# Kernel optimization log

Measured on AMD Instinct MI355X. Metric: run time of the kernel, lower is better.

## Reference

```python
import jax, jax.numpy as jnp
import numpy as np

EPS = 1e-5  # torch LayerNorm default

def _layer_norm(v, w, b):
    mu = jnp.mean(v, axis=-1, keepdims=True)
    var = jnp.mean(jnp.square(v - mu), axis=-1, keepdims=True)
    return (v - mu) * jax.lax.rsqrt(var + EPS) * w + b

def _gru_layer(x, h0, w_ih, b_ih, w_hh, b_hh, ln_w, ln_b):
    # x: [B,T,in], h0: [B,H]
    H = h0.shape[-1]
    # precompute input gates for whole sequence: [B,T,3H]
    x_gates = jnp.einsum('bti,gi->btg', x, w_ih) + b_ih

    def step(h, xg_t):
        hg = jnp.einsum('bh,gh->bg', h, w_hh) + b_hh
        x_r, x_z, x_n = jnp.split(xg_t, 3, axis=-1)
        h_r, h_z, h_n = jnp.split(hg, 3, axis=-1)
        r = jax.nn.sigmoid(_layer_norm(x_r + h_r, ln_w[0], ln_b[0]))
        z = jax.nn.sigmoid(_layer_norm(x_z + h_z, ln_w[1], ln_b[1]))
        n = jnp.tanh(_layer_norm(x_n + r * h_n, ln_w[2], ln_b[2]))
        h_new = (1 - z) * n + z * h
        return h_new, h_new

    h_final, ys = jax.lax.scan(step, h0, jnp.swapaxes(x_gates, 0, 1))
    return jnp.swapaxes(ys, 0, 1), h_final  # [B,T,H], [B,H]

def setup_inputs() -> dict:
    key = jax.random.key(0)
    ks = jax.random.split(key, 4)
    B, T, D, H, L = 64, 512, 768, 768, 2
    G = 3 * H
    x = jax.random.normal(ks[0], (B, T, D), dtype=jnp.float32)
    h_0 = jnp.zeros((L, B, H), dtype=jnp.float32)
    # scaled gaussian stands in for orthogonal init
    w_ih = jax.random.normal(ks[1], (L, G, D), dtype=jnp.float32) / np.sqrt(D)
    w_hh = jax.random.normal(ks[2], (L, G, H), dtype=jnp.float32) / np.sqrt(H)
    b_ih = jnp.zeros((L, G), dtype=jnp.float32)
    b_hh = jnp.zeros((L, G), dtype=jnp.float32)
    ln_w = jnp.ones((L, 3, H), dtype=jnp.float32)
    ln_b = jnp.zeros((L, 3, H), dtype=jnp.float32)
    return {"x": x, "h_0": h_0, "w_ih": w_ih, "b_ih": b_ih,
            "w_hh": w_hh, "b_hh": b_hh, "ln_w": ln_w, "ln_b": ln_b}

def reference(x, h_0, w_ih, b_ih, w_hh, b_hh, ln_w, ln_b):
    num_layers = h_0.shape[0]
    layer_output = x
    x_residual = x  # input_size == hidden_size -> identity residual
    finals = []
    for i in range(num_layers):
        seq, h_fin = _gru_layer(layer_output, h_0[i], w_ih[i], b_ih[i],
                                w_hh[i], b_hh[i], ln_w[i], ln_b[i])
        if i == 0:
            seq = seq + x_residual
        else:
            seq = seq + layer_output
        layer_output = seq  # dropout=0.0, eval mode -> no-op
        finals.append(h_fin)
    h_final_stack = jnp.stack(finals, axis=0)
    return layer_output, h_final_stack
```

## Files before the change

kernel.cpp:

```cpp
#include <hip/hip_runtime.h>

typedef short bf16x8 __attribute__((ext_vector_type(8)));
typedef float f32x4 __attribute__((ext_vector_type(4)));

__device__ __forceinline__ unsigned pack2bf(float a, float b) {
  union { float f; unsigned u; } x, y;
  x.f = a; y.f = b;
  unsigned ra = (x.u + 0x7FFFu + ((x.u >> 16) & 1u)) >> 16;
  unsigned rb = (y.u + 0x7FFFu + ((y.u >> 16) & 1u)) & 0xFFFF0000u;
  return ra | rb;
}
__device__ __forceinline__ unsigned short bfu(float f) {
  union { float f; unsigned u; } v; v.f = f;
  return (unsigned short)((v.u + 0x7FFFu + ((v.u >> 16) & 1u)) >> 16);
}
__device__ __forceinline__ float sigf(float x) { return 1.f / (1.f + __expf(-x)); }

#define KB 64
#define LDSP 72

__global__ __launch_bounds__(256) void gemm_bt(
    const float* __restrict__ A0, size_t a_bstride,
    const float* __restrict__ W,
    const float* __restrict__ bias,
    float* __restrict__ out, size_t o_bstride,
    int Mvalid)
{
  __shared__ unsigned short As[64][LDSP];
  __shared__ unsigned short Bs[64][LDSP];
  const int tid = threadIdx.x;
  const int g0 = blockIdx.x * 64;
  const int mlo = blockIdx.z * 64;
  const float* Ab = A0 + (size_t)blockIdx.y * a_bstride + (size_t)mlo * 768;
  float* outb = out + (size_t)blockIdx.y * o_bstride + (size_t)mlo * 2304;

  const int srow = tid >> 2;
  const int scol = (tid & 3) << 4;
  const int wv = tid >> 6;
  const int lane = tid & 63;
  const int wr = wv >> 1, wc = wv & 1;
  const int lrow = lane & 15;
  const int lk = (lane >> 4) << 3;

  f32x4 acc[2][2];
#pragma unroll
  for (int i = 0; i < 2; ++i)
#pragma unroll
    for (int j = 0; j < 2; ++j)
      acc[i][j] = (f32x4){0.f, 0.f, 0.f, 0.f};

  const float* Aptr = Ab + (size_t)srow * 768 + scol;
  const float* Bptr = W + ((size_t)(g0 + srow)) * 768 + scol;
  const bool aval = (mlo + srow) < Mvalid;

  for (int k0 = 0; k0 < 768; k0 += KB) {
    uint4 ua0, ua1, ub0, ub1;
    if (aval) {
      const float4* qa = (const float4*)(Aptr + k0);
      float4 f0 = qa[0], f1 = qa[1], f2 = qa[2], f3 = qa[3];
      ua0 = make_uint4(pack2bf(f0.x, f0.y), pack2bf(f0.z, f0.w),
                       pack2bf(f1.x, f1.y), pack2bf(f1.z, f1.w));
      ua1 = make_uint4(pack2bf(f2.x, f2.y), pack2bf(f2.z, f2.w),
                       pack2bf(f3.x, f3.y), pack2bf(f3.z, f3.w));
    } else {
      ua0 = make_uint4(0u, 0u, 0u, 0u);
      ua1 = ua0;
    }
    {
      const float4* qb = (const float4*)(Bptr + k0);
      float4 f0 = qb[0], f1 = qb[1], f2 = qb[2], f3 = qb[3];
      ub0 = make_uint4(pack2bf(f0.x, f0.y), pack2bf(f0.z, f0.w),
                       pack2bf(f1.x, f1.y), pack2bf(f1.z, f1.w));
      ub1 = make_uint4(pack2bf(f2.x, f2.y), pack2bf(f2.z, f2.w),
                       pack2bf(f3.x, f3.y), pack2bf(f3.z, f3.w));
    }
    __syncthreads();
    *(uint4*)&As[srow][scol] = ua0;
    *(uint4*)&As[srow][scol + 8] = ua1;
    *(uint4*)&Bs[srow][scol] = ub0;
    *(uint4*)&Bs[srow][scol + 8] = ub1;
    __syncthreads();
#pragma unroll
    for (int kh = 0; kh < 2; ++kh) {
      bf16x8 a0 = *(const bf16x8*)&As[32 * wr + lrow][32 * kh + lk];
      bf16x8 a1 = *(const bf16x8*)&As[32 * wr + 16 + lrow][32 * kh + lk];
      bf16x8 b0 = *(const bf16x8*)&Bs[32 * wc + lrow][32 * kh + lk];
      bf16x8 b1 = *(const bf16x8*)&Bs[32 * wc + 16 + lrow][32 * kh + lk];
      acc[0][0] = __builtin_amdgcn_mfma_f32_16x16x32_bf16(a0, b0, acc[0][0], 0, 0, 0);
      acc[0][1] = __builtin_amdgcn_mfma_f32_16x16x32_bf16(a0, b1, acc[0][1], 0, 0, 0);
      acc[1][0] = __builtin_amdgcn_mfma_f32_16x16x32_bf16(a1, b0, acc[1][0], 0, 0, 0);
      acc[1][1] = __builtin_amdgcn_mfma_f32_16x16x32_bf16(a1, b1, acc[1][1], 0, 0, 0);
    }
  }

  const int lgrp = lane >> 4;
#pragma unroll
  for (int fr = 0; fr < 2; ++fr)
#pragma unroll
    for (int fc = 0; fc < 2; ++fc)
#pragma unroll
      for (int j = 0; j < 4; ++j) {
        int m = 32 * wr + 16 * fr + lgrp * 4 + j;
        int n = 32 * wc + 16 * fc + lrow;
        if (mlo + m < Mvalid)
          outb[(size_t)m * 2304 + g0 + n] = acc[fr][fc][j] + bias[g0 + n];
      }
}

#define NWGP 72
#define NWGC 64
#define NWGT 136
#define EPS 1e-5f
#define INV768 (1.0f / 768.0f)
#define SLOT 24576u

__device__ __forceinline__ void bar_arrive(unsigned* c) {
  __syncthreads();
  if (threadIdx.x == 0)
    __hip_atomic_fetch_add(c + (blockIdx.x & 7) * 32, 1u,
                           __ATOMIC_RELAXED, __HIP_MEMORY_SCOPE_AGENT);
}
__device__ __forceinline__ void bar_wait(unsigned* c, unsigned tgt) {
  if (threadIdx.x == 0) {
    for (;;) {
      unsigned s = 0;
#pragma unroll
      for (int i = 0; i < 8; ++i)
        s += __hip_atomic_load(c + i * 32, __ATOMIC_RELAXED, __HIP_MEMORY_SCOPE_AGENT);
      if (s >= tgt) break;
      __builtin_amdgcn_s_sleep(1);
    }
  }
  __syncthreads();
}

template <int N>
__device__ __forceinline__ void blk_reduce(float* v, float* lds) {
#pragma unroll
  for (int k = 0; k < N; ++k) {
    float x = v[k];
#pragma unroll
    for (int off = 1; off < 64; off <<= 1) x += __shfl_xor(x, off);
    v[k] = x;
  }
  const int wv = threadIdx.x >> 6;
  const int lane = threadIdx.x & 63;
  if (lane == 0) {
#pragma unroll
    for (int k = 0; k < N; ++k) lds[wv * N + k] = v[k];
  }
  __syncthreads();
#pragma unroll
  for (int k = 0; k < N; ++k)
    v[k] = lds[k] + lds[N + k] + lds[2 * N + k] + lds[3 * N + k];
  __syncthreads();
}

#define WAITV(n) do { asm volatile("s_waitcnt vmcnt(" #n ")" ::: "memory"); \
                      __builtin_amdgcn_sched_barrier(0); } while (0)

#define LD24(buf, base) \
  { _Pragma("unroll") for (int kk_ = 0; kk_ < 24; ++kk_) { \
      const unsigned* p_ = (base) + (size_t)kk_ * 1024u; \
      asm volatile("global_load_dwordx4 %0, %1, off sc0 sc1" : "=v"(buf[kk_]) : "v"(p_)); } }

#define WRRING(ring, t, val) \
  { unsigned* rp_ = (ring) + (unsigned)(((t) & 3)) * SLOT; \
    _Pragma("unroll") for (int p_ = 0; p_ < 3; ++p_) { \
      int i_ = tid + (p_ << 8); \
      float other_ = __shfl_xor(val[p_], 1); \
      if ((tid & 1) == 0) { \
        unsigned pk_ = pack2bf(val[p_], other_); \
        __hip_atomic_store(rp_ + (i_ >> 3) * 256 + b * 4 + ((i_ >> 1) & 3), pk_, \
                           __ATOMIC_RELAXED, __HIP_MEMORY_SCOPE_AGENT); } } }

__global__ __launch_bounds__(256, 1) void gru_super(
    const float* __restrict__ Whh1, const float* __restrict__ bhh1,
    const float* __restrict__ Wih2, const float* __restrict__ bih2,
    const float* __restrict__ Whh2, const float* __restrict__ bhh2,
    const float* __restrict__ lnw, const float* __restrict__ lnb,
    const float* __restrict__ x,
    const float* __restrict__ xg1,
    int t0, int TC,
    const float* __restrict__ h0,
    float* __restrict__ hstate,
    unsigned* __restrict__ h1ring, unsigned* __restrict__ s1ring,
    unsigned* __restrict__ h2ring,
    float* __restrict__ hg1, float* __restrict__ xg2, float* __restrict__ hg2,
    unsigned* __restrict__ bar,
    float* __restrict__ seq,
    float* __restrict__ hfin,
    int firstflag, int lastflag)
{
  __shared__ unsigned short Wl[96][776];
  __shared__ float bl96[96];
  __shared__ float redl[32];

  unsigned* barA = bar;
  unsigned* barB = bar + 512;

  const int wg = blockIdx.x;
  const int tid = threadIdx.x;
  const int lane = tid & 63;
  const int w = tid >> 6;
  const int la = lane & 15;
  const int kb = lane >> 4;
  const int arow = 16 * w + la;

  if (wg < NWGP) {
    const int mcls = wg / 24;
    const int g0w = (wg % 24) * 96;
    const unsigned abase = (unsigned)((kb * 64 + arow) << 2);
    {
      const float* Wsrc = (mcls == 0) ? Whh1 : (mcls == 1) ? Wih2 : Whh2;
      const float* bsrc = (mcls == 0) ? bhh1 : (mcls == 1) ? bih2 : bhh2;
      for (int r = 0; r < 96; ++r) {
        const float* src = Wsrc + (size_t)(g0w + r) * 768;
        for (int c = tid; c < 768; c += 256) Wl[r][c] = bfu(src[c]);
      }
      if (tid < 96) bl96[tid] = bsrc[g0w + tid];
    }
    float* dst = (mcls == 0) ? hg1 : (mcls == 1) ? xg2 : hg2;

    for (int s = 0; s <= TC; ++s) {
      const int t1 = t0 + s;
      const bool active = (mcls == 0) ? (s < TC) : (s >= 1);
      bar_wait(barB, 64u * (unsigned)(s + 1));
      if (active) {
        const unsigned* rbase =
            (mcls == 0) ? (h1ring + (unsigned)((t1 - 1) & 3) * SLOT)
          : (mcls == 1) ? (s1ring + (unsigned)((t1 - 1) & 3) * SLOT)
                        : (h2ring + (unsigned)((t1 - 2) & 3) * SLOT);
        const unsigned* hb = rbase + abase;
        f32x4 acc[6];
#pragma unroll
        for (int r = 0; r < 6; ++r) acc[r] = (f32x4){0.f, 0.f, 0.f, 0.f};
        bf16x8 buf[24];
        LD24(buf, hb);
        WAITV(0);
#pragma unroll
        for (int kk = 0; kk < 24; ++kk) {
#pragma unroll
          for (int r = 0; r < 6; ++r) {
            bf16x8 wv2 = *(const bf16x8*)&Wl[16 * r + la][kk * 32 + kb * 8];
            acc[r] = __builtin_amdgcn_mfma_f32_16x16x32_bf16(buf[kk], wv2, acc[r], 0, 0, 0);
          }
        }
#pragma unroll
        for (int r = 0; r < 6; ++r)
#pragma unroll
          for (int j = 0; j < 4; ++j) {
            int bb = 16 * w + kb * 4 + j;
            __hip_atomic_store(dst + (size_t)bb * 2304 + g0w + 16 * r + la,
                               acc[r][j] + bl96[16 * r + la],
                               __ATOMIC_RELAXED, __HIP_MEMORY_SCOPE_AGENT);
          }
      }
      bar_arrive(barA);
    }
    return;
  }

  const int b = wg - NWGP;
  float hreg1[3], hreg2[3];
  float h1prev[3], xprev[3] = {0.f, 0.f, 0.f}, xcur[3] = {0.f, 0.f, 0.f};
  float lw1[9], lb1[9], lw2[9], lb2[9];
#pragma unroll
  for (int g = 0; g < 3; ++g)
#pragma unroll
    for (int p = 0; p < 3; ++p) {
      int idx = g * 3 + p, gi = g * 768 + tid + (p << 8);
      lw1[idx] = lnw[gi];          lb1[idx] = lnb[gi];
      lw2[idx] = lnw[2304 + gi];   lb2[idx] = lnb[2304 + gi];
    }
#pragma unroll
  for (int p = 0; p < 3; ++p) {
    int i = tid + (p << 8);
    hreg1[p] = firstflag ? h0[(size_t)b * 768 + i] : hstate[(size_t)b * 768 + i];
    hreg2[p] = firstflag ? h0[49152 + (size_t)b * 768 + i] : hstate[49152 + (size_t)b * 768 + i];
    h1prev[p] = hreg1[p];
  }
  if (firstflag) {
    WRRING(h1ring, 3, hreg1);
    WRRING(h2ring, 3, hreg2);
  }
  bar_arrive(barB);

  for (int s = 0; s <= TC; ++s) {
    const int t1 = t0 + s;
    const bool doL1 = (s < TC);
    const bool doL2 = (s >= 1);

    const int ttc = doL1 ? s : (TC - 1);
    float x1v[9];
    {
      const float* xg1b = xg1 + ((size_t)b * TC + ttc) * 2304;
#pragma unroll
      for (int p = 0; p < 9; ++p) x1v[p] = xg1b[tid + p * 256];
    }
    if (doL1) {
#pragma unroll
      for (int p = 0; p < 3; ++p)
        xcur[p] = x[((size_t)b * 512 + t1) * 768 + tid + (p << 8)];
    }

    bar_wait(barA, 72u * (unsigned)(s + 1));

    float g1v[9], g2v[9], g3v[9];
    {
      const float* p1 = hg1 + (size_t)b * 2304;
      const float* p2 = xg2 + (size_t)b * 2304;
      const float* p3 = hg2 + (size_t)b * 2304;
#pragma unroll
      for (int p = 0; p < 9; ++p) {
        const float* q1 = p1 + tid + p * 256;
        const float* q2 = p2 + tid + p * 256;
        const float* q3 = p3 + tid + p * 256;
        asm volatile("global_load_dword %0, %1, off sc0 sc1" : "=v"(g1v[p]) : "v"(q1));
        asm volatile("global_load_dword %0, %1, off sc0 sc1" : "=v"(g2v[p]) : "v"(q2));
        asm volatile("global_load_dword %0, %1, off sc0 sc1" : "=v"(g3v[p]) : "v"(q3));
      }
    }
    WAITV(0);

    float s11[3], s21[3], s12[3], s22[3];
    float v8[8] = {0,0,0,0,0,0,0,0};
#pragma unroll
    for (int p = 0; p < 3; ++p) {
      s11[p] = g1v[p] + x1v[p];
      s21[p] = g1v[3 + p] + x1v[3 + p];
      s12[p] = g2v[p] + g3v[p];
      s22[p] = g2v[3 + p] + g3v[3 + p];
      v8[0] += s11[p]; v8[1] += s11[p] * s11[p];
      v8[2] += s21[p]; v8[3] += s21[p] * s21[p];
      v8[4] += s12[p]; v8[5] += s12[p] * s12[p];
      v8[6] += s22[p]; v8[7] += s22[p] * s22[p];
    }
    blk_reduce<8>(v8, redl);
    float mu11 = v8[0] * INV768, rs11 = rsqrtf(v8[1] * INV768 - mu11 * mu11 + EPS);
    float mu21 = v8[2] * INV768, rs21 = rsqrtf(v8[3] * INV768 - mu21 * mu21 + EPS);
    float mu12 = v8[4] * INV768, rs12 = rsqrtf(v8[5] * INV768 - mu12 * mu12 + EPS);
    float mu22 = v8[6] * INV768, rs22 = rsqrtf(v8[7] * INV768 - mu22 * mu22 + EPS);

    float z1[3], m1[3], z2[3], m2[3];
    float v4[4] = {0,0,0,0};
#pragma unroll
    for (int p = 0; p < 3; ++p) {
      float r1 = sigf((s11[p] - mu11) * rs11 * lw1[p] + lb1[p]);
      z1[p]    = sigf((s21[p] - mu21) * rs21 * lw1[3 + p] + lb1[3 + p]);
      m1[p] = x1v[6 + p] + r1 * g1v[6 + p];
      float r2 = sigf((s12[p] - mu12) * rs12 * lw2[p] + lb2[p]);
      z2[p]    = sigf((s22[p] - mu22) * rs22 * lw2[3 + p] + lb2[3 + p]);
      m2[p] = g2v[6 + p] + r2 * g3v[6 + p];
      v4[0] += m1[p]; v4[1] += m1[p] * m1[p];
      v4[2] += m2[p]; v4[3] += m2[p] * m2[p];
    }
    blk_reduce<4>(v4, redl);
    float mum1 = v4[0] * INV768, rsm1 = rsqrtf(v4[1] * INV768 - mum1 * mum1 + EPS);
    float mum2 = v4[2] * INV768, rsm2 = rsqrtf(v4[3] * INV768 - mum2 * mum2 + EPS);

    float h1new[3], s1new[3], h2new[3], seqv[3];
#pragma unroll
    for (int p = 0; p < 3; ++p) {
      float n1 = tanhf((m1[p] - mum1) * rsm1 * lw1[6 + p] + lb1[6 + p]);
      h1new[p] = (1.f - z1[p]) * n1 + z1[p] * hreg1[p];
      s1new[p] = h1new[p] + xcur[p];
      float n2 = tanhf((m2[p] - mum2) * rsm2 * lw2[6 + p] + lb2[6 + p]);
      h2new[p] = (1.f - z2[p]) * n2 + z2[p] * hreg2[p];
    }
    if (doL2) {
#pragma unroll
      for (int p = 0; p < 3; ++p) {
        hreg2[p] = h2new[p];
        seqv[p] = h2new[p] + h1prev[p] + xprev[p];
      }
      WRRING(h2ring, t1 - 1, h2new);
    }
    if (doL1) {
#pragma unroll
      for (int p = 0; p < 3; ++p) {
        hreg1[p] = h1new[p];
        h1prev[p] = h1new[p];
        xprev[p] = xcur[p];
      }
      WRRING(h1ring, t1, h1new);
      WRRING(s1ring, t1, s1new);
    }
    bar_arrive(barB);
    if (doL2) {
      const int t2 = t1 - 1;
#pragma unroll
      for (int p = 0; p < 3; ++p) {
        int i = tid + (p << 8);
        seq[((size_t)b * 512 + t2) * 768 + i] = seqv[p];
      }
    }
  }

#pragma unroll
  for (int p = 0; p < 3; ++p) {
    int i = tid + (p << 8);
    hstate[(size_t)b * 768 + i] = hreg1[p];
    hstate[49152 + (size_t)b * 768 + i] = hreg2[p];
    if (lastflag) {
      hfin[(size_t)b * 768 + i] = hreg1[p];
      hfin[49152 + (size_t)b * 768 + i] = hreg2[p];
    }
  }
}

extern "C" void kernel_launch(void* const* d_in, const int* in_sizes, int n_in,
                              void* d_out, int out_size, void* d_ws, size_t ws_size,
                              hipStream_t stream) {
  const float* x    = (const float*)d_in[0];
  const float* h0   = (const float*)d_in[1];
  const float* w_ih = (const float*)d_in[2];
  const float* b_ih = (const float*)d_in[3];
  const float* w_hh = (const float*)d_in[4];
  const float* b_hh = (const float*)d_in[5];
  const float* lnw  = (const float*)d_in[6];
  const float* lnb  = (const float*)d_in[7];
  float* out = (float*)d_out;

  const int B = 64, T = 512, H = 768, G = 2304;

  const size_t BAR = 65536;
  const size_t RING = 4u * SLOT * 4u;
  const size_t HGB = (size_t)B * G * 4;
  int CHUNK = 128;
  for (;;) {
    size_t need = BAR + 3 * RING + 3 * HGB + 2 * (size_t)B * H * 4
                + (size_t)B * CHUNK * G * 4;
    if (need <= ws_size || CHUNK == 8) break;
    CHUNK >>= 1;
  }

  char* wp = (char*)d_ws;
  unsigned* barctr = (unsigned*)wp;            wp += BAR;
  unsigned* h1ring = (unsigned*)wp;            wp += RING;
  unsigned* s1ring = (unsigned*)wp;            wp += RING;
  unsigned* h2ring = (unsigned*)wp;            wp += RING;
  float* hg1 = (float*)wp;                     wp += HGB;
  float* xg2 = (float*)wp;                     wp += HGB;
  float* hg2 = (float*)wp;                     wp += HGB;
  float* hstate = (float*)wp;                  wp += 2 * (size_t)B * H * 4;
  float* xg1 = (float*)wp;

  hipMemsetAsync(barctr, 0, BAR, stream);

  float* seq  = out;
  float* hfin = out + (size_t)B * T * H;
  const int NCH = T / CHUNK;

  const float* Wih1 = w_ih;
  const float* Wih2 = w_ih + (size_t)G * H;
  const float* Whh1 = w_hh;
  const float* Whh2 = w_hh + (size_t)G * H;

  for (int c = 0; c < NCH; ++c) {
    int t0 = c * CHUNK;
    gemm_bt<<<dim3(G / 64, B, CHUNK / 64), 256, 0, stream>>>(
        x + (size_t)t0 * H, (size_t)T * H, Wih1, b_ih,
        xg1, (size_t)CHUNK * G, CHUNK);
    gru_super<<<NWGT, 256, 0, stream>>>(
        Whh1, b_hh, Wih2, b_ih + G, Whh2, b_hh + G,
        lnw, lnb, x, xg1, t0, CHUNK,
        h0, hstate, h1ring, s1ring, h2ring,
        hg1, xg2, hg2,
        barctr + (size_t)c * 1024,
        seq, hfin,
        (c == 0) ? 1 : 0, (c == NCH - 1) ? 1 : 0);
  }
}
```

Before: 6.639 ms.

## Split layer-1 and layer-2 cell workgroups into separate per-batch blocks

The persistent kernel now launches 200 workgroups. The 64 cell workgroups that each handled both layers for one batch row become 128: 64 handle layer 1 and 64 handle layer 2, and the barrier target rises to 128 arrivals. Each cell block now runs half the elementwise and LayerNorm work per step with smaller reductions, which should shorten the critical path between the grid barriers. In exchange, layer-2 blocks read the layer-1 output plus residual back from the bf16 s1ring instead of summing fp32 values in registers, which lowers precision of the residual, and more blocks take part in each barrier.

```diff
diff --git a/kernel.cpp b/kernel.cpp
--- a/kernel.cpp
+++ b/kernel.cpp
@@ -13,6 +13,9 @@
 __device__ __forceinline__ unsigned short bfu(float f) {
   union { float f; unsigned u; } v; v.f = f;
   return (unsigned short)((v.u + 0x7FFFu + ((v.u >> 16) & 1u)) >> 16);
+}
+__device__ __forceinline__ float u2f(unsigned u) {
+  union { unsigned u; float f; } v; v.u = u; return v.f;
 }
 __device__ __forceinline__ float sigf(float x) { return 1.f / (1.f + __expf(-x)); }
 
@@ -107,9 +110,7 @@
       }
 }
 
-#define NWGP 72
-#define NWGC 64
-#define NWGT 136
+#define NWGT 200
 #define EPS 1e-5f
 #define INV768 (1.0f / 768.0f)
 #define SLOT 24576u
@@ -207,7 +208,7 @@
   const int kb = lane >> 4;
   const int arow = 16 * w + la;
 
-  if (wg < NWGP) {
+  if (wg < 72) {
     const int mcls = wg / 24;
     const int g0w = (wg % 24) * 96;
     const unsigned abase = (unsigned)((kb * 64 + arow) << 2);
@@ -224,8 +225,10 @@
 
     for (int s = 0; s <= TC; ++s) {
       const int t1 = t0 + s;
-      const bool active = (mcls == 0) ? (s < TC) : (s >= 1);
-      bar_wait(barB, 64u * (unsigned)(s + 1));
+      const bool doL1 = (s < TC);
+      const bool doL2 = (s >= 1);
+      const bool active = (mcls == 0) ? doL1 : doL2;
+      bar_wait(barB, 128u * (unsigned)(s + 1));
       if (active) {
         const unsigned* rbase =
             (mcls == 0) ? (h1ring + (unsigned)((t1 - 1) & 3) * SLOT)
@@ -234,25 +237,25 @@
         const unsigned* hb = rbase + abase;
         f32x4 acc[6];
 #pragma unroll
-        for (int r = 0; r < 6; ++r) acc[r] = (f32x4){0.f, 0.f, 0.f, 0.f};
+        for (int q = 0; q < 6; ++q) acc[q] = (f32x4){0.f, 0.f, 0.f, 0.f};
         bf16x8 buf[24];
         LD24(buf, hb);
         WAITV(0);
 #pragma unroll
         for (int kk = 0; kk < 24; ++kk) {
 #pragma unroll
-          for (int r = 0; r < 6; ++r) {
-            bf16x8 wv2 = *(const bf16x8*)&Wl[16 * r + la][kk * 32 + kb * 8];
-            acc[r] = __builtin_amdgcn_mfma_f32_16x16x32_bf16(buf[kk], wv2, acc[r], 0, 0, 0);
+          for (int q = 0; q < 6; ++q) {
+            bf16x8 wv2 = *(const bf16x8*)&Wl[16 * q + la][kk * 32 + kb * 8];
+            acc[q] = __builtin_amdgcn_mfma_f32_16x16x32_bf16(buf[kk], wv2, acc[q], 0, 0, 0);
           }
         }
 #pragma unroll
-        for (int r = 0; r < 6; ++r)
+        for (int q = 0; q < 6; ++q)
 #pragma unroll
           for (int j = 0; j < 4; ++j) {
             int bb = 16 * w + kb * 4 + j;
-            __hip_atomic_store(dst + (size_t)bb * 2304 + g0w + 16 * r + la,
-                               acc[r][j] + bl96[16 * r + la],
+            __hip_atomic_store(dst + (size_t)bb * 2304 + g0w + 16 * q + la,
+                               acc[q][j] + bl96[16 * q + la],
                                __ATOMIC_RELAXED, __HIP_MEMORY_SCOPE_AGENT);
           }
       }
@@ -261,150 +264,201 @@
     return;
   }
 
-  const int b = wg - NWGP;
-  float hreg1[3], hreg2[3];
-  float h1prev[3], xprev[3] = {0.f, 0.f, 0.f}, xcur[3] = {0.f, 0.f, 0.f};
-  float lw1[9], lb1[9], lw2[9], lb2[9];
-#pragma unroll
-  for (int g = 0; g < 3; ++g)
+  if (wg < 136) {
+    const int b = wg - 72;
+    float hreg1[3], lw1[9], lb1[9];
+#pragma unroll
+    for (int g = 0; g < 3; ++g)
+#pragma unroll
+      for (int p = 0; p < 3; ++p) {
+        int gi = g * 768 + tid + (p << 8);
+        lw1[g * 3 + p] = lnw[gi];  lb1[g * 3 + p] = lnb[gi];
+      }
 #pragma unroll
     for (int p = 0; p < 3; ++p) {
-      int idx = g * 3 + p, gi = g * 768 + tid + (p << 8);
-      lw1[idx] = lnw[gi];          lb1[idx] = lnb[gi];
-      lw2[idx] = lnw[2304 + gi];   lb2[idx] = lnb[2304 + gi];
-    }
-#pragma unroll
-  for (int p = 0; p < 3; ++p) {
-    int i = tid + (p << 8);
-    hreg1[p] = firstflag ? h0[(size_t)b * 768 + i] : hstate[(size_t)b * 768 + i];
-    hreg2[p] = firstflag ? h0[49152 + (size_t)b * 768 + i] : hstate[49152 + (size_t)b * 768 + i];
-    h1prev[p] = hreg1[p];
-  }
-  if (firstflag) {
+      int i = tid + (p << 8);
+      hreg1[p] = firstflag ? h0[(size_t)b * 768 + i] : hstate[(size_t)b * 768 + i];
+    }
     WRRING(h1ring, 3, hreg1);
+    bar_arrive(barB);
+
+    for (int s = 0; s <= TC; ++s) {
+      const int t1 = t0 + s;
+      const bool doL1 = (s < TC);
+      float x1v[9], xcur[3];
+      if (doL1) {
+        const float* xg1b = xg1 + ((size_t)b * TC + s) * 2304;
+#pragma unroll
+        for (int p = 0; p < 9; ++p) x1v[p] = xg1b[tid + p * 256];
+#pragma unroll
+        for (int p = 0; p < 3; ++p)
+          xcur[p] = x[((size_t)b * 512 + t1) * 768 + tid + (p << 8)];
+      }
+      bar_wait(barA, 72u * (unsigned)(s + 1));
+
+      if (doL1) {
+        float g1v[9];
+        {
+          const float* p1 = hg1 + (size_t)b * 2304;
+#pragma unroll
+          for (int p = 0; p < 9; ++p) {
+            const float* q1 = p1 + tid + p * 256;
+            asm volatile("global_load_dword %0, %1, off sc0 sc1" : "=v"(g1v[p]) : "v"(q1));
+          }
+        }
+        WAITV(0);
+
+        float s11[3], s21[3];
+        float v4[4] = {0, 0, 0, 0};
+#pragma unroll
+        for (int p = 0; p < 3; ++p) {
+          s11[p] = g1v[p] + x1v[p];
+          s21[p] = g1v[3 + p] + x1v[3 + p];
+          v4[0] += s11[p]; v4[1] += s11[p] * s11[p];
+          v4[2] += s21[p]; v4[3] += s21[p] * s21[p];
+        }
+        blk_reduce<4>(v4, redl);
+        float mu1 = v4[0] * INV768, rs1 = rsqrtf(v4[1] * INV768 - mu1 * mu1 + EPS);
+        float mu2 = v4[2] * INV768, rs2 = rsqrtf(v4[3] * INV768 - mu2 * mu2 + EPS);
+
+        float z1[3], m1[3];
+        float v2[2] = {0, 0};
+#pragma unroll
+        for (int p = 0; p < 3; ++p) {
+          float r1 = sigf((s11[p] - mu1) * rs1 * lw1[p] + lb1[p]);
+          z1[p]    = sigf((s21[p] - mu2) * rs2 * lw1[3 + p] + lb1[3 + p]);
+          m1[p] = x1v[6 + p] + r1 * g1v[6 + p];
+          v2[0] += m1[p]; v2[1] += m1[p] * m1[p];
+        }
+        blk_reduce<2>(v2, redl);
+        float mum = v2[0] * INV768, rsm = rsqrtf(v2[1] * INV768 - mum * mum + EPS);
+
+        float h1new[3], s1new[3];
+#pragma unroll
+        for (int p = 0; p < 3; ++p) {
+          float n1 = tanhf((m1[p] - mum) * rsm * lw1[6 + p] + lb1[6 + p]);
+          h1new[p] = (1.f - z1[p]) * n1 + z1[p] * hreg1[p];
+          s1new[p] = h1new[p] + xcur[p];
+          hreg1[p] = h1new[p];
+        }
+        WRRING(h1ring, t1, h1new);
+        WRRING(s1ring, t1, s1new);
+      }
+      bar_arrive(barB);
+    }
+
+#pragma unroll
+    for (int p = 0; p < 3; ++p) {
+      int i = tid + (p << 8);
+      hstate[(size_t)b * 768 + i] = hreg1[p];
+      if (lastflag) hfin[(size_t)b * 768 + i] = hreg1[p];
+    }
+    return;
+  }
+
+  {
+    const int b = wg - 136;
+    float hreg2[3], lw2[9], lb2[9];
+#pragma unroll
+    for (int g = 0; g < 3; ++g)
+#pragma unroll
+      for (int p = 0; p < 3; ++p) {
+        int gi = 2304 + g * 768 + tid + (p << 8);
+        lw2[g * 3 + p] = lnw[gi];  lb2[g * 3 + p] = lnb[gi];
+      }
+#pragma unroll
+    for (int p = 0; p < 3; ++p) {
+      int i = tid + (p << 8);
+      hreg2[p] = firstflag ? h0[49152 + (size_t)b * 768 + i]
+                           : hstate[49152 + (size_t)b * 768 + i];
+    }
     WRRING(h2ring, 3, hreg2);
-  }
-  bar_arrive(barB);
-
-  for (int s = 0; s <= TC; ++s) {
-    const int t1 = t0 + s;
-    const bool doL1 = (s < TC);
-    const bool doL2 = (s >= 1);
-
-    const int ttc = doL1 ? s : (TC - 1);
-    float x1v[9];
-    {
-      const float* xg1b = xg1 + ((size_t)b * TC + ttc) * 2304;
-#pragma unroll
-      for (int p = 0; p < 9; ++p) x1v[p] = xg1b[tid + p * 256];
-    }
-    if (doL1) {
-#pragma unroll
-      for (int p = 0; p < 3; ++p)
-        xcur[p] = x[((size_t)b * 512 + t1) * 768 + tid + (p << 8)];
-    }
-
-    bar_wait(barA, 72u * (unsigned)(s + 1));
-
-    float g1v[9], g2v[9], g3v[9];
-    {
-      const float* p1 = hg1 + (size_t)b * 2304;
-      const float* p2 = xg2 + (size_t)b * 2304;
-      const float* p3 = hg2 + (size_t)b * 2304;
-#pragma unroll
-      for (int p = 0; p < 9; ++p) {
-        const float* q1 = p1 + tid + p * 256;
-        const float* q2 = p2 + tid + p * 256;
-        const float* q3 = p3 + tid + p * 256;
-        asm volatile("global_load_dword %0, %1, off sc0 sc1" : "=v"(g1v[p]) : "v"(q1));
-        asm volatile("global_load_dword %0, %1, off sc0 sc1" : "=v"(g2v[p]) : "v"(q2));
-        asm volatile("global_load_dword %0, %1, off sc0 sc1" : "=v"(g3v[p]) : "v"(q3));
-      }
-    }
-    WAITV(0);
-
-    float s11[3], s21[3], s12[3], s22[3];
-    float v8[8] = {0,0,0,0,0,0,0,0};
+    bar_arrive(barB);
+
+    for (int s = 0; s <= TC; ++s) {
+      const bool doL2 = (s >= 1);
+      const int t2 = t0 + s - 1;
+      bar_wait(barA, 72u * (unsigned)(s + 1));
+
+      float seqv[3];
+      if (doL2) {
+        float g2v[9], g3v[9];
+        unsigned s1raw[3];
+        {
+          const float* p2 = xg2 + (size_t)b * 2304;
+          const float* p3 = hg2 + (size_t)b * 2304;
+#pragma unroll
+          for (int p = 0; p < 9; ++p) {
+            const float* q2 = p2 + tid + p * 256;
+            const float* q3 = p3 + tid + p * 256;
+            asm volatile("global_load_dword %0, %1, off sc0 sc1" : "=v"(g2v[p]) : "v"(q2));
+            asm volatile("global_load_dword %0, %1, off sc0 sc1" : "=v"(g3v[p]) : "v"(q3));
+          }
+          const unsigned* rp = s1ring + (unsigned)(t2 & 3) * SLOT;
+#pragma unroll
+          for (int p = 0; p < 3; ++p) {
+            int i = tid + (p << 8);
+            const unsigned* qs = rp + (i >> 3) * 256 + b * 4 + ((i >> 1) & 3);
+            asm volatile("global_load_dword %0, %1, off sc0 sc1" : "=v"(s1raw[p]) : "v"(qs));
+          }
+        }
+        WAITV(0);
+        float s1v[3];
+        const bool hi = (tid & 1);
+#pragma unroll
+        for (int p = 0; p < 3; ++p)
+          s1v[p] = hi ? u2f(s1raw[p] & 0xFFFF0000u) : u2f(s1raw[p] << 16);
+
+        float s12[3], s22[3];
+        float v4[4] = {0, 0, 0, 0};
+#pragma unroll
+        for (int p = 0; p < 3; ++p) {
+          s12[p] = g2v[p] + g3v[p];
+          s22[p] = g2v[3 + p] + g3v[3 + p];
+          v4[0] += s12[p]; v4[1] += s12[p] * s12[p];
+          v4[2] += s22[p]; v4[3] += s22[p] * s22[p];
+        }
+        blk_reduce<4>(v4, redl);
+        float mu1 = v4[0] * INV768, rs1 = rsqrtf(v4[1] * INV768 - mu1 * mu1 + EPS);
+        float mu2 = v4[2] * INV768, rs2 = rsqrtf(v4[3] * INV768 - mu2 * mu2 + EPS);
+
+        float z2[3], m2[3];
+        float v2[2] = {0, 0};
+#pragma unroll
+        for (int p = 0; p < 3; ++p) {
+          float r2 = sigf((s12[p] - mu1) * rs1 * lw2[p] + lb2[p]);
+          z2[p]    = sigf((s22[p] - mu2) * rs2 * lw2[3 + p] + lb2[3 + p]);
+          m2[p] = g2v[6 + p] + r2 * g3v[6 + p];
+          v2[0] += m2[p]; v2[1] += m2[p] * m2[p];
+        }
+        blk_reduce<2>(v2, redl);
+        float mum = v2[0] * INV768, rsm = rsqrtf(v2[1] * INV768 - mum * mum + EPS);
+
+        float h2new[3];
+#pragma unroll
+        for (int p = 0; p < 3; ++p) {
+          float n2 = tanhf((m2[p] - mum) * rsm * lw2[6 + p] + lb2[6 + p]);
+          h2new[p] = (1.f - z2[p]) * n2 + z2[p] * hreg2[p];
+          hreg2[p] = h2new[p];
+          seqv[p] = h2new[p] + s1v[p];
+        }
+        WRRING(h2ring, t2, h2new);
+      }
+      bar_arrive(barB);
+      if (doL2) {
+#pragma unroll
+        for (int p = 0; p < 3; ++p) {
+          int i = tid + (p << 8);
+          seq[((size_t)b * 512 + t2) * 768 + i] = seqv[p];
+        }
+      }
+    }
+
 #pragma unroll
     for (int p = 0; p < 3; ++p) {
-      s11[p] = g1v[p] + x1v[p];
-      s21[p] = g1v[3 + p] + x1v[3 + p];
-      s12[p] = g2v[p] + g3v[p];
-      s22[p] = g2v[3 + p] + g3v[3 + p];
-      v8[0] += s11[p]; v8[1] += s11[p] * s11[p];
-      v8[2] += s21[p]; v8[3] += s21[p] * s21[p];
-      v8[4] += s12[p]; v8[5] += s12[p] * s12[p];
-      v8[6] += s22[p]; v8[7] += s22[p] * s22[p];
-    }
-    blk_reduce<8>(v8, redl);
-    float mu11 = v8[0] * INV768, rs11 = rsqrtf(v8[1] * INV768 - mu11 * mu11 + EPS);
-    float mu21 = v8[2] * INV768, rs21 = rsqrtf(v8[3] * INV768 - mu21 * mu21 + EPS);
-    float mu12 = v8[4] * INV768, rs12 = rsqrtf(v8[5] * INV768 - mu12 * mu12 + EPS);
-    float mu22 = v8[6] * INV768, rs22 = rsqrtf(v8[7] * INV768 - mu22 * mu22 + EPS);
-
-    float z1[3], m1[3], z2[3], m2[3];
-    float v4[4] = {0,0,0,0};
-#pragma unroll
-    for (int p = 0; p < 3; ++p) {
-      float r1 = sigf((s11[p] - mu11) * rs11 * lw1[p] + lb1[p]);
-      z1[p]    = sigf((s21[p] - mu21) * rs21 * lw1[3 + p] + lb1[3 + p]);
-      m1[p] = x1v[6 + p] + r1 * g1v[6 + p];
-      float r2 = sigf((s12[p] - mu12) * rs12 * lw2[p] + lb2[p]);
-      z2[p]    = sigf((s22[p] - mu22) * rs22 * lw2[3 + p] + lb2[3 + p]);
-      m2[p] = g2v[6 + p] + r2 * g3v[6 + p];
-      v4[0] += m1[p]; v4[1] += m1[p] * m1[p];
-      v4[2] += m2[p]; v4[3] += m2[p] * m2[p];
-    }
-    blk_reduce<4>(v4, redl);
-    float mum1 = v4[0] * INV768, rsm1 = rsqrtf(v4[1] * INV768 - mum1 * mum1 + EPS);
-    float mum2 = v4[2] * INV768, rsm2 = rsqrtf(v4[3] * INV768 - mum2 * mum2 + EPS);
-
-    float h1new[3], s1new[3], h2new[3], seqv[3];
-#pragma unroll
-    for (int p = 0; p < 3; ++p) {
-      float n1 = tanhf((m1[p] - mum1) * rsm1 * lw1[6 + p] + lb1[6 + p]);
-      h1new[p] = (1.f - z1[p]) * n1 + z1[p] * hreg1[p];
-      s1new[p] = h1new[p] + xcur[p];
-      float n2 = tanhf((m2[p] - mum2) * rsm2 * lw2[6 + p] + lb2[6 + p]);
-      h2new[p] = (1.f - z2[p]) * n2 + z2[p] * hreg2[p];
-    }
-    if (doL2) {
-#pragma unroll
-      for (int p = 0; p < 3; ++p) {
-        hreg2[p] = h2new[p];
-        seqv[p] = h2new[p] + h1prev[p] + xprev[p];
-      }
-      WRRING(h2ring, t1 - 1, h2new);
-    }
-    if (doL1) {
-#pragma unroll
-      for (int p = 0; p < 3; ++p) {
-        hreg1[p] = h1new[p];
-        h1prev[p] = h1new[p];
-        xprev[p] = xcur[p];
-      }
-      WRRING(h1ring, t1, h1new);
-      WRRING(s1ring, t1, s1new);
-    }
-    bar_arrive(barB);
-    if (doL2) {
-      const int t2 = t1 - 1;
-#pragma unroll
-      for (int p = 0; p < 3; ++p) {
-        int i = tid + (p << 8);
-        seq[((size_t)b * 512 + t2) * 768 + i] = seqv[p];
-      }
-    }
-  }
-
-#pragma unroll
-  for (int p = 0; p < 3; ++p) {
-    int i = tid + (p << 8);
-    hstate[(size_t)b * 768 + i] = hreg1[p];
-    hstate[49152 + (size_t)b * 768 + i] = hreg2[p];
-    if (lastflag) {
-      hfin[(size_t)b * 768 + i] = hreg1[p];
-      hfin[49152 + (size_t)b * 768 + i] = hreg2[p];
+      int i = tid + (p << 8);
+      hstate[49152 + (size_t)b * 768 + i] = hreg2[p];
+      if (lastflag) hfin[49152 + (size_t)b * 768 + i] = hreg2[p];
     }
   }
 }
```

Result: faster. 6.499 ms (-2.1%).
